# Kernel optimization log

Hardware: AMD Instinct MI355X
Metric: run time of the kernel (lower is better)

Reference implementation:

```python
import jax, jax.numpy as jnp
import numpy as np

B, S, K, DEPTH = 8, 8192, 512, 2
NUM_SPECIALS = 4  # bos, eos, pad, eop


def setup_inputs() -> dict:
    key = jax.random.key(0)
    ks = jax.random.split(key, 6)
    stage_logits = jax.random.normal(ks[0], (DEPTH, B, S, K), jnp.float32)
    special_logits = jax.random.normal(ks[1], (B, S, NUM_SPECIALS), jnp.float32)
    seq = jax.random.randint(ks[2], (B, S), 0, K ** DEPTH, jnp.int32)
    lengths = jax.random.randint(ks[3], (B,), S // 2, S)
    kpm = jnp.arange(S)[None, :] >= lengths[:, None]              # True = pad
    end_mask = (jax.random.uniform(ks[4], (B, S)) < 0.1) & (~kpm)  # segment ends
    # exclusive cumsum of end_mask -> segment ids
    seg = jnp.cumsum(
        jnp.pad(end_mask[:, :-1], ((0, 0), (1, 0))).astype(jnp.int32), axis=1)
    targets = jax.random.randint(ks[5], (B, S), 0, K ** DEPTH + NUM_SPECIALS, jnp.int32)
    return {
        "stage_logits": stage_logits,
        "special_logits": special_logits,
        "seq": seq,
        "end_mask": end_mask,
        "kpm": kpm,
        "seg": seg,
        "targets": targets,
        "tgt_kpm": kpm,
        "eop_id": K ** DEPTH + 3,
        "pad_id": K ** DEPTH + 2,
    }


def _insert_eop(seq, end_mask, kpm, seg, eop_id, pad_id):
    """Length-preserving EOP insertion + seg-id update (torch _insert_eop_fixed_len_with_seg)."""
    B_, S_ = seq.shape
    pad_slots = kpm.sum(axis=1)                                   # free slots per row
    csum = jnp.cumsum(end_mask.astype(jnp.int32), axis=1)
    end_mask = end_mask & (csum <= pad_slots[:, None])            # cap insertions by capacity
    m = end_mask.astype(jnp.int32)
    c = jnp.cumsum(m, axis=1)
    shift = c - m                                                  # inclusive-cumsum minus self
    real = ~kpm
    tok = jnp.arange(S_, dtype=jnp.int32)[None, :]
    bidx = jnp.arange(B_)[:, None]
    tgt = tok + shift                                              # destination of each real token
    tgt_real = jnp.where(real, tgt, S_)                            # index S_ -> dropped (OOB)
    out = jnp.full((B_, S_), pad_id, seq.dtype)
    out = out.at[bidx, tgt_real].set(seq, mode="drop")
    out_kpm = jnp.ones((B_, S_), bool).at[bidx, tgt_real].set(False, mode="drop")
    out_seg = jnp.zeros_like(seg).at[bidx, tgt_real].set(seg, mode="drop")
    need_eop = real & end_mask
    tgt_eop = jnp.where(need_eop, tgt + 1, S_)                     # EOP right after the token
    out = out.at[bidx, tgt_eop].set(eop_id, mode="drop")
    out_kpm = out_kpm.at[bidx, tgt_eop].set(False, mode="drop")
    out_seg = out_seg.at[bidx, tgt_eop].set(seg, mode="drop")      # EOP inherits seg id
    last_seg = jnp.clip(jnp.max(jnp.where(kpm, -1, seg), axis=1), 0, None)
    out_seg = jnp.where(out_kpm, last_seg[:, None], out_seg)       # pads get last seg id
    return out, out_kpm, out_seg


def _factorized_ce(stage_logits, special_logits, targets, tgt_kpm):
    """Stage-wise digit CE + special-head CE (torch _factorized_code_ce with codec)."""
    depth, _, _, Kd = stage_logits.shape
    base = Kd ** depth
    is_special = targets >= base
    valid = (~is_special) & (~tgt_kpm)
    denom = jnp.maximum(valid.sum(), 1).astype(stage_logits.dtype)
    digit_loss = jnp.zeros((), stage_logits.dtype)
    for s in range(depth):  # small fixed loop over VQ stages
        dig = (targets // (Kd ** s)) % Kd                          # codec.decompose digit s
        logp = jax.nn.log_softmax(stage_logits[s], axis=-1)
        ce = -jnp.take_along_axis(logp, dig[..., None], axis=-1)[..., 0]
        digit_loss = digit_loss + (ce * valid).sum() / denom
    sp_local = jnp.clip(targets - base, 0, special_logits.shape[-1] - 1)
    sp_mask = is_special & (~tgt_kpm)
    logp_sp = jax.nn.log_softmax(special_logits, axis=-1)
    ce_sp = -jnp.take_along_axis(logp_sp, sp_local[..., None], axis=-1)[..., 0]
    special_loss = (ce_sp * sp_mask).sum() / jnp.maximum(sp_mask.sum(), 1).astype(ce_sp.dtype)
    return digit_loss, special_loss


def reference(stage_logits, special_logits, seq, end_mask, kpm, seg, targets, tgt_kpm, eop_id, pad_id):
    out, out_kpm, out_seg = _insert_eop(seq, end_mask, kpm, seg, eop_id, pad_id)
    digit_ce, special_ce = _factorized_ce(stage_logits, special_logits, targets, tgt_kpm)
    return out, out_kpm, out_seg, digit_ce, special_ce
```

## Files before the change

### kernel.cpp

```cpp
#include <hip/hip_runtime.h>

#define S_LEN 8192
#define B_SZ 8
#define BASE 262144
#define BT_TOTAL 65536
#define ROWS_TOTAL 131072
#define EOP_BLOCKS 8
#define CE_BLOCKS 504
#define GRID_TOTAL 512
#define CE_WAVES (CE_BLOCKS * 16)


__device__ __forceinline__ int load_bool(const void* p, int idx, int isByte) {
  return isByte ? (int)((const unsigned char*)p)[idx] : ((const int*)p)[idx];
}

__global__ __launch_bounds__(1024, 8) void fused_kernel(
    const float* __restrict__ stage_logits,
    const float* __restrict__ sp_logits,
    const int* __restrict__ seq,
    const void* __restrict__ end_mask,
    const void* __restrict__ kpm,
    const int* __restrict__ seg,
    const int* __restrict__ targets,
    const void* __restrict__ tgt_kpm,
    const int* __restrict__ eop_idp,
    const int* __restrict__ pad_idp,
    float* __restrict__ out,
    float* __restrict__ wsf, int* __restrict__ wsi) {
  __shared__ int s_seg[S_LEN];
  __shared__ float s_red[16];
  __shared__ int s_redi[16];
  __shared__ int sh_w[16], sh_ps[16], sh_ls[16];
  __shared__ int sh_pad, sh_last, sh_carry;

  const int tid = threadIdx.x;
  const int lane = tid & 63;
  const int wid = tid >> 6;

  const int isByte = ((((const unsigned*)kpm)[2047] & ~1u) != 0u) ? 1 : 0;

  if (blockIdx.x >= EOP_BLOCKS) {
    const int g = (blockIdx.x - EOP_BLOCKS) * 16 + wid;

    int tgt_l = 0, val_l = 0;
    {
      const int r_l = g + lane * CE_WAVES;
      if (lane < 17 && r_l < ROWS_TOTAL) {
        const int bt = r_l & (BT_TOTAL - 1);
        tgt_l = targets[bt];
        const int kp = load_bool(tgt_kpm, bt, isByte);
        val_l = (!kp && tgt_l < BASE) ? 1 : 0;
      }
    }

    float ce_sum = 0.f;
    int vcnt = 0;
    int n = 0;
    for (int r = g; r < ROWS_TOTAL; r += CE_WAVES, ++n) {
      const int v = __shfl(val_l, n);
      if (!v) continue;
      const int tgt = __shfl(tgt_l, n);
      const int stage = r >> 16;

      const float* rowp = stage_logits + ((size_t)r << 9);
      const float4 c0 = ((const float4*)rowp)[lane];
      const float4 c1 = ((const float4*)rowp)[lane + 64];

      float ssum = __expf(c0.x) + __expf(c0.y) + __expf(c0.z) + __expf(c0.w) +
                   __expf(c1.x) + __expf(c1.y) + __expf(c1.z) + __expf(c1.w);
      for (int off = 32; off; off >>= 1) ssum += __shfl_xor(ssum, off);

      const int dig = stage ? (tgt >> 9) : (tgt & 511);
      const int srcLane = (dig >> 2) & 63;
      const int j = dig & 3;
      float xv;
      if (dig < 256)
        xv = (j == 0) ? c0.x : (j == 1) ? c0.y : (j == 2) ? c0.z : c0.w;
      else
        xv = (j == 0) ? c1.x : (j == 1) ? c1.y : (j == 2) ? c1.z : c1.w;
      xv = __shfl(xv, srcLane);

      ce_sum += __logf(ssum) - xv;
      vcnt += (stage == 0);
    }

    if (lane == 0) { s_red[wid] = ce_sum; s_redi[wid] = vcnt; }
    __syncthreads();
    if (tid == 0) {
      float a = 0.f;
      int c = 0;
      for (int i = 0; i < 16; ++i) { a += s_red[i]; c += s_redi[i]; }
      atomicAdd(&wsf[0], a);
      if (c) atomicAdd(&wsi[2], c);
    }
  } else {
    const int b = blockIdx.x;
    const int eop_id = eop_idp[0];
    const int pad_id = pad_idp[0];

    float* outF = out + (size_t)b * S_LEN;
    float* kpmF = out + BT_TOTAL + (size_t)b * S_LEN;
    float* segF = out + 2 * BT_TOTAL + (size_t)b * S_LEN;
    const int* seqR = seq + (size_t)b * S_LEN;
    const int* segR = seg + (size_t)b * S_LEN;
    const int rowBase = b * S_LEN;

    for (int t = tid; t < S_LEN; t += 1024) {
      outF[t] = (float)pad_id;
      s_seg[t] = -1;
    }

    int ps = 0, ls = -1;
    for (int t = tid; t < S_LEN; t += 1024) {
      const int kp = load_bool(kpm, rowBase + t, isByte);
      ps += kp;
      if (!kp) ls = max(ls, segR[t]);
    }
    for (int off = 32; off; off >>= 1) {
      ps += __shfl_xor(ps, off);
      ls = max(ls, __shfl_xor(ls, off));
    }
    if (lane == 0) { sh_ps[wid] = ps; sh_ls[wid] = ls; }
    __syncthreads();
    if (tid == 0) {
      int a = 0, m = -1;
      for (int i = 0; i < 16; ++i) { a += sh_ps[i]; m = max(m, sh_ls[i]); }
      sh_pad = a;
      sh_last = max(m, 0);
      sh_carry = 0;
    }
    __syncthreads();
    const int pad_slots = sh_pad;
    const int last_seg = sh_last;

    for (int tile = 0; tile < 8; ++tile) {
      const int t = tile * 1024 + tid;
      const int e = load_bool(end_mask, rowBase + t, isByte);
      int x = e;
      for (int off = 1; off < 64; off <<= 1) {
        const int y = __shfl_up(x, off);
        if (lane >= off) x += y;
      }
      if (lane == 63) sh_w[wid] = x;
      __syncthreads();
      if (tid == 0) {
        int acc = sh_carry;
        for (int i = 0; i < 16; ++i) { const int v = sh_w[i]; sh_w[i] = acc; acc += v; }
        sh_carry = acc;
      }
      __syncthreads();
      const int csum_raw = sh_w[wid] + x;
      const int em2 = (e && csum_raw <= pad_slots) ? 1 : 0;
      const int c = min(csum_raw, pad_slots);
      const int shift = c - em2;
      const int kp = load_bool(kpm, rowBase + t, isByte);
      if (!kp) {
        const int tgt = t + shift;
        const int sv = segR[t];
        if (tgt < S_LEN) {
          outF[tgt] = (float)seqR[t];
          s_seg[tgt] = sv;
        }
        if (em2 && (tgt + 1) < S_LEN) {
          outF[tgt + 1] = (float)eop_id;
          s_seg[tgt + 1] = sv;
        }
      }
      __syncthreads();
    }

    for (int t = tid; t < S_LEN; t += 1024) {
      const int sv = s_seg[t];
      kpmF[t] = (sv < 0) ? 1.0f : 0.0f;
      segF[t] = (sv < 0) ? (float)last_seg : (float)sv;
    }

    float sp_sum = 0.f;
    int sp_cnt = 0;
    for (int t = tid; t < S_LEN; t += 1024) {
      const int bt = rowBase + t;
      const int tgt = targets[bt];
      const int kp = load_bool(tgt_kpm, bt, isByte);
      if (!kp && tgt >= BASE) {
        const float4 v = ((const float4*)sp_logits)[bt];
        const float m = fmaxf(fmaxf(v.x, v.y), fmaxf(v.z, v.w));
        const float ssum = __expf(v.x - m) + __expf(v.y - m) +
                           __expf(v.z - m) + __expf(v.w - m);
        const int sl = min(tgt - BASE, 3);
        const float xv = (sl == 0) ? v.x : (sl == 1) ? v.y
                        : (sl == 2) ? v.z : v.w;
        sp_sum += m + __logf(ssum) - xv;
        ++sp_cnt;
      }
    }
    for (int off = 32; off; off >>= 1) {
      sp_sum += __shfl_xor(sp_sum, off);
      sp_cnt += __shfl_xor(sp_cnt, off);
    }
    if (lane == 0) { s_red[wid] = sp_sum; s_redi[wid] = sp_cnt; }
    __syncthreads();
    if (tid == 0) {
      float a = 0.f;
      int c = 0;
      for (int i = 0; i < 16; ++i) { a += s_red[i]; c += s_redi[i]; }
      if (a != 0.f) atomicAdd(&wsf[1], a);
      if (c) atomicAdd(&wsi[3], c);
    }
  }

  __syncthreads();
  if (tid == 0) {
    __threadfence();
    const int old = atomicAdd(&wsi[4], 1);
    if (old == GRID_TOTAL - 1) {
      __threadfence();
      const float ds = __hip_atomic_load(&wsf[0], __ATOMIC_RELAXED,
                                         __HIP_MEMORY_SCOPE_AGENT);
      const float ss = __hip_atomic_load(&wsf[1], __ATOMIC_RELAXED,
                                         __HIP_MEMORY_SCOPE_AGENT);
      const int vc = __hip_atomic_load(&wsi[2], __ATOMIC_RELAXED,
                                       __HIP_MEMORY_SCOPE_AGENT);
      const int sc = __hip_atomic_load(&wsi[3], __ATOMIC_RELAXED,
                                       __HIP_MEMORY_SCOPE_AGENT);
      out[3 * BT_TOTAL] = ds / (float)max(vc, 1);
      out[3 * BT_TOTAL + 1] = ss / (float)max(sc, 1);
    }
  }
}

extern "C" void kernel_launch(void* const* d_in, const int* in_sizes, int n_in,
                              void* d_out, int out_size, void* d_ws,
                              size_t ws_size, hipStream_t stream) {
  const float* stage_logits   = (const float*)d_in[0];
  const float* special_logits = (const float*)d_in[1];
  const int*   seq            = (const int*)d_in[2];
  const void*  end_mask       = d_in[3];
  const void*  kpm            = d_in[4];
  const int*   seg            = (const int*)d_in[5];
  const int*   targets        = (const int*)d_in[6];
  const void*  tgt_kpm        = d_in[7];
  const int*   eop_idp        = (const int*)d_in[8];
  const int*   pad_idp        = (const int*)d_in[9];

  hipMemsetAsync(d_ws, 0, 64, stream);
  fused_kernel<<<GRID_TOTAL, 1024, 0, stream>>>(
      stage_logits, special_logits, seq, end_mask, kpm, seg, targets, tgt_kpm,
      eop_idp, pad_idp, (float*)d_out, (float*)d_ws, (int*)d_ws);
}
```

Measured before the change: 387.8 us.

## Process both stages per token and software-pipeline row loads in CE waves

Each CE wave now iterates over token positions, not stage rows, and loads the stage-0 and stage-1 logit rows for the same token together, so targets and validity are read once per token. Valid tokens are enumerated with a ballot mask and ctz, which skips invalid tokens without a per-row branch. The loads for the next valid token are issued before the current token's shuffle reductions, overlapping memory latency with compute. This costs extra registers for the double row buffers.

```diff
diff --git a/kernel.cpp b/kernel.cpp
--- a/kernel.cpp
+++ b/kernel.cpp
@@ -45,44 +45,74 @@
 
     int tgt_l = 0, val_l = 0;
     {
-      const int r_l = g + lane * CE_WAVES;
-      if (lane < 17 && r_l < ROWS_TOTAL) {
-        const int bt = r_l & (BT_TOTAL - 1);
-        tgt_l = targets[bt];
-        const int kp = load_bool(tgt_kpm, bt, isByte);
+      const int bt_l = g + lane * CE_WAVES;
+      if (lane < 9 && bt_l < BT_TOTAL) {
+        tgt_l = targets[bt_l];
+        const int kp = load_bool(tgt_kpm, bt_l, isByte);
         val_l = (!kp && tgt_l < BASE) ? 1 : 0;
       }
     }
+    unsigned long long m = __ballot(val_l);
+    const int vcnt = __popcll(m);
 
     float ce_sum = 0.f;
-    int vcnt = 0;
-    int n = 0;
-    for (int r = g; r < ROWS_TOTAL; r += CE_WAVES, ++n) {
-      const int v = __shfl(val_l, n);
-      if (!v) continue;
-      const int tgt = __shfl(tgt_l, n);
-      const int stage = r >> 16;
-
-      const float* rowp = stage_logits + ((size_t)r << 9);
-      const float4 c0 = ((const float4*)rowp)[lane];
-      const float4 c1 = ((const float4*)rowp)[lane + 64];
-
-      float ssum = __expf(c0.x) + __expf(c0.y) + __expf(c0.z) + __expf(c0.w) +
-                   __expf(c1.x) + __expf(c1.y) + __expf(c1.z) + __expf(c1.w);
-      for (int off = 32; off; off >>= 1) ssum += __shfl_xor(ssum, off);
-
-      const int dig = stage ? (tgt >> 9) : (tgt & 511);
-      const int srcLane = (dig >> 2) & 63;
-      const int j = dig & 3;
-      float xv;
-      if (dig < 256)
-        xv = (j == 0) ? c0.x : (j == 1) ? c0.y : (j == 2) ? c0.z : c0.w;
-      else
-        xv = (j == 0) ? c1.x : (j == 1) ? c1.y : (j == 2) ? c1.z : c1.w;
-      xv = __shfl(xv, srcLane);
-
-      ce_sum += __logf(ssum) - xv;
-      vcnt += (stage == 0);
+    if (m) {
+      float4 a0, a1, b0, b1;
+      auto issue = [&](int n) {
+        const size_t bt = (size_t)(g + n * CE_WAVES);
+        const float4* p0 = (const float4*)(stage_logits + (bt << 9));
+        const float4* p1 =
+            (const float4*)(stage_logits + ((bt + BT_TOTAL) << 9));
+        a0 = p0[lane];
+        a1 = p0[lane + 64];
+        b0 = p1[lane];
+        b1 = p1[lane + 64];
+      };
+
+      int n = __builtin_ctzll(m);
+      m &= m - 1;
+      issue(n);
+      int tgt = __shfl(tgt_l, n);
+
+      while (true) {
+        float s0 = __expf(a0.x) + __expf(a0.y) + __expf(a0.z) + __expf(a0.w) +
+                   __expf(a1.x) + __expf(a1.y) + __expf(a1.z) + __expf(a1.w);
+        float s1 = __expf(b0.x) + __expf(b0.y) + __expf(b0.z) + __expf(b0.w) +
+                   __expf(b1.x) + __expf(b1.y) + __expf(b1.z) + __expf(b1.w);
+
+        const int d0 = tgt & 511;
+        const int d1 = tgt >> 9;
+        const int j0 = d0 & 3, j1 = d1 & 3;
+        float x0 = (d0 < 256)
+            ? ((j0 == 0) ? a0.x : (j0 == 1) ? a0.y : (j0 == 2) ? a0.z : a0.w)
+            : ((j0 == 0) ? a1.x : (j0 == 1) ? a1.y : (j0 == 2) ? a1.z : a1.w);
+        float x1 = (d1 < 256)
+            ? ((j1 == 0) ? b0.x : (j1 == 1) ? b0.y : (j1 == 2) ? b0.z : b0.w)
+            : ((j1 == 0) ? b1.x : (j1 == 1) ? b1.y : (j1 == 2) ? b1.z : b1.w);
+        const int src0 = (d0 >> 2) & 63;
+        const int src1 = (d1 >> 2) & 63;
+
+        const bool more = (m != 0);
+        int tgtN = 0;
+        if (more) {
+          const int n2 = __builtin_ctzll(m);
+          m &= m - 1;
+          issue(n2);
+          tgtN = __shfl(tgt_l, n2);
+        }
+
+#pragma unroll
+        for (int off = 32; off; off >>= 1) {
+          s0 += __shfl_xor(s0, off);
+          s1 += __shfl_xor(s1, off);
+        }
+        x0 = __shfl(x0, src0);
+        x1 = __shfl(x1, src1);
+        ce_sum += (__logf(s0) - x0) + (__logf(s1) - x1);
+
+        if (!more) break;
+        tgt = tgtN;
+      }
     }
 
     if (lane == 0) { s_red[wid] = ce_sum; s_redi[wid] = vcnt; }
@@ -124,10 +154,10 @@
     if (lane == 0) { sh_ps[wid] = ps; sh_ls[wid] = ls; }
     __syncthreads();
     if (tid == 0) {
-      int a = 0, m = -1;
-      for (int i = 0; i < 16; ++i) { a += sh_ps[i]; m = max(m, sh_ls[i]); }
+      int a = 0, mx = -1;
+      for (int i = 0; i < 16; ++i) { a += sh_ps[i]; mx = max(mx, sh_ls[i]); }
       sh_pad = a;
-      sh_last = max(m, 0);
+      sh_last = max(mx, 0);
       sh_carry = 0;
     }
     __syncthreads();
@@ -184,13 +214,13 @@
       const int kp = load_bool(tgt_kpm, bt, isByte);
       if (!kp && tgt >= BASE) {
         const float4 v = ((const float4*)sp_logits)[bt];
-        const float m = fmaxf(fmaxf(v.x, v.y), fmaxf(v.z, v.w));
-        const float ssum = __expf(v.x - m) + __expf(v.y - m) +
-                           __expf(v.z - m) + __expf(v.w - m);
+        const float mx = fmaxf(fmaxf(v.x, v.y), fmaxf(v.z, v.w));
+        const float ssum = __expf(v.x - mx) + __expf(v.y - mx) +
+                           __expf(v.z - mx) + __expf(v.w - mx);
         const int sl = min(tgt - BASE, 3);
         const float xv = (sl == 0) ? v.x : (sl == 1) ? v.y
                         : (sl == 2) ? v.z : v.w;
-        sp_sum += m + __logf(ssum) - xv;
+        sp_sum += mx + __logf(ssum) - xv;
         ++sp_cnt;
       }
     }
```

New measurement: 391.2 us. No clear change (+0.9%).

## Compact CE work to non-padded rows via prefix-sum and prefetch next row

Applied to the files above, without the earlier changes.

The CE blocks now binary-search each batch row's padding length in tgt_kpm, which assumes padding is a contiguous suffix. They build a prefix sum of valid row counts over both stages and give each block a contiguous chunk of non-pad rows, replacing the strided loop that tested validity per row. The loop also software-pipelines the next row's logits and target load while reducing the current row. The intent is to balance load across blocks and cut wasted iterations on pad rows, at the cost of relying on the suffix-pad layout of the mask.

```diff
diff --git a/kernel.cpp b/kernel.cpp
--- a/kernel.cpp
+++ b/kernel.cpp
@@ -8,7 +8,6 @@
 #define EOP_BLOCKS 8
 #define CE_BLOCKS 504
 #define GRID_TOTAL 512
-#define CE_WAVES (CE_BLOCKS * 16)
 
 
 __device__ __forceinline__ int load_bool(const void* p, int idx, int isByte) {
@@ -33,6 +32,8 @@
   __shared__ int s_redi[16];
   __shared__ int sh_w[16], sh_ps[16], sh_ls[16];
   __shared__ int sh_pad, sh_last, sh_carry;
+  __shared__ int sh_len[8];
+  __shared__ int sh_P[17];
 
   const int tid = threadIdx.x;
   const int lane = tid & 63;
@@ -41,48 +42,86 @@
   const int isByte = ((((const unsigned*)kpm)[2047] & ~1u) != 0u) ? 1 : 0;
 
   if (blockIdx.x >= EOP_BLOCKS) {
-    const int g = (blockIdx.x - EOP_BLOCKS) * 16 + wid;
-
-    int tgt_l = 0, val_l = 0;
-    {
-      const int r_l = g + lane * CE_WAVES;
-      if (lane < 17 && r_l < ROWS_TOTAL) {
-        const int bt = r_l & (BT_TOTAL - 1);
-        tgt_l = targets[bt];
-        const int kp = load_bool(tgt_kpm, bt, isByte);
-        val_l = (!kp && tgt_l < BASE) ? 1 : 0;
-      }
-    }
+    if (tid < 8) {
+      int lo = 0, hi = S_LEN;
+      while (lo < hi) {
+        const int mid = (lo + hi) >> 1;
+        if (load_bool(tgt_kpm, tid * S_LEN + mid, isByte)) hi = mid;
+        else lo = mid + 1;
+      }
+      sh_len[tid] = lo;
+    }
+    __syncthreads();
+    if (tid == 0) {
+      int acc = 0;
+      for (int i = 0; i < 16; ++i) { sh_P[i] = acc; acc += sh_len[i & 7]; }
+      sh_P[16] = acc;
+    }
+    __syncthreads();
+
+    const int Rv = sh_P[16];
+    const int C = (Rv + CE_BLOCKS - 1) / CE_BLOCKS;
+    const int cb = blockIdx.x - EOP_BLOCKS;
+    int v = cb * C + wid;
+    const int v1 = min(cb * C + C, Rv);
 
     float ce_sum = 0.f;
     int vcnt = 0;
-    int n = 0;
-    for (int r = g; r < ROWS_TOTAL; r += CE_WAVES, ++n) {
-      const int v = __shfl(val_l, n);
-      if (!v) continue;
-      const int tgt = __shfl(tgt_l, n);
-      const int stage = r >> 16;
-
-      const float* rowp = stage_logits + ((size_t)r << 9);
-      const float4 c0 = ((const float4*)rowp)[lane];
-      const float4 c1 = ((const float4*)rowp)[lane + 64];
+    int j = 0;
+    float4 c0, c1;
+    int tgtC = 0, sC = 0;
+
+    if (v < v1) {
+      while (v >= sh_P[j + 1]) ++j;
+      const int t = v - sh_P[j];
+      const int bb = j & 7;
+      sC = j >> 3;
+      const float* rowp =
+          stage_logits +
+          ((((size_t)sC << 16) + ((size_t)bb << 13) + (size_t)t) << 9);
+      c0 = ((const float4*)rowp)[lane];
+      c1 = ((const float4*)rowp)[lane + 64];
+      tgtC = targets[(bb << 13) + t];
+    }
+
+    while (v < v1) {
+      const int vn = v + 16;
+      const bool more = vn < v1;
+      float4 n0, n1;
+      int tgtN = 0, sN = 0;
+      if (more) {
+        while (vn >= sh_P[j + 1]) ++j;
+        const int t = vn - sh_P[j];
+        const int bb = j & 7;
+        sN = j >> 3;
+        const float* rowp =
+            stage_logits +
+            ((((size_t)sN << 16) + ((size_t)bb << 13) + (size_t)t) << 9);
+        n0 = ((const float4*)rowp)[lane];
+        n1 = ((const float4*)rowp)[lane + 64];
+        tgtN = targets[(bb << 13) + t];
+      }
 
       float ssum = __expf(c0.x) + __expf(c0.y) + __expf(c0.z) + __expf(c0.w) +
                    __expf(c1.x) + __expf(c1.y) + __expf(c1.z) + __expf(c1.w);
+
+      const int dig = sC ? (tgtC >> 9) : (tgtC & 511);
+      const int jj = dig & 3;
+      float xv = (dig < 256)
+          ? ((jj == 0) ? c0.x : (jj == 1) ? c0.y : (jj == 2) ? c0.z : c0.w)
+          : ((jj == 0) ? c1.x : (jj == 1) ? c1.y : (jj == 2) ? c1.z : c1.w);
+
+#pragma unroll
       for (int off = 32; off; off >>= 1) ssum += __shfl_xor(ssum, off);
-
-      const int dig = stage ? (tgt >> 9) : (tgt & 511);
-      const int srcLane = (dig >> 2) & 63;
-      const int j = dig & 3;
-      float xv;
-      if (dig < 256)
-        xv = (j == 0) ? c0.x : (j == 1) ? c0.y : (j == 2) ? c0.z : c0.w;
-      else
-        xv = (j == 0) ? c1.x : (j == 1) ? c1.y : (j == 2) ? c1.z : c1.w;
-      xv = __shfl(xv, srcLane);
-
-      ce_sum += __logf(ssum) - xv;
-      vcnt += (stage == 0);
+      xv = __shfl(xv, (dig >> 2) & 63);
+
+      if (tgtC < BASE) {
+        ce_sum += __logf(ssum) - xv;
+        vcnt += (sC == 0) ? 1 : 0;
+      }
+
+      v = vn;
+      if (more) { c0 = n0; c1 = n1; tgtC = tgtN; sC = sN; }
     }
 
     if (lane == 0) { s_red[wid] = ce_sum; s_redi[wid] = vcnt; }
@@ -124,10 +163,10 @@
     if (lane == 0) { sh_ps[wid] = ps; sh_ls[wid] = ls; }
     __syncthreads();
     if (tid == 0) {
-      int a = 0, m = -1;
-      for (int i = 0; i < 16; ++i) { a += sh_ps[i]; m = max(m, sh_ls[i]); }
+      int a = 0, mx = -1;
+      for (int i = 0; i < 16; ++i) { a += sh_ps[i]; mx = max(mx, sh_ls[i]); }
       sh_pad = a;
-      sh_last = max(m, 0);
+      sh_last = max(mx, 0);
       sh_carry = 0;
     }
     __syncthreads();
@@ -146,7 +185,7 @@
       __syncthreads();
       if (tid == 0) {
         int acc = sh_carry;
-        for (int i = 0; i < 16; ++i) { const int v = sh_w[i]; sh_w[i] = acc; acc += v; }
+        for (int i = 0; i < 16; ++i) { const int vv = sh_w[i]; sh_w[i] = acc; acc += vv; }
         sh_carry = acc;
       }
       __syncthreads();
@@ -183,14 +222,14 @@
       const int tgt = targets[bt];
       const int kp = load_bool(tgt_kpm, bt, isByte);
       if (!kp && tgt >= BASE) {
-        const float4 v = ((const float4*)sp_logits)[bt];
-        const float m = fmaxf(fmaxf(v.x, v.y), fmaxf(v.z, v.w));
-        const float ssum = __expf(v.x - m) + __expf(v.y - m) +
-                           __expf(v.z - m) + __expf(v.w - m);
+        const float4 vv = ((const float4*)sp_logits)[bt];
+        const float mx = fmaxf(fmaxf(vv.x, vv.y), fmaxf(vv.z, vv.w));
+        const float ssum = __expf(vv.x - mx) + __expf(vv.y - mx) +
+                           __expf(vv.z - mx) + __expf(vv.w - mx);
         const int sl = min(tgt - BASE, 3);
-        const float xv = (sl == 0) ? v.x : (sl == 1) ? v.y
-                        : (sl == 2) ? v.z : v.w;
-        sp_sum += m + __logf(ssum) - xv;
+        const float xv = (sl == 0) ? vv.x : (sl == 1) ? vv.y
+                        : (sl == 2) ? vv.z : vv.w;
+        sp_sum += mx + __logf(ssum) - xv;
         ++sp_cnt;
       }
     }
```

New measurement: 391.4 us. About the same (+0.9%).
